# Performance work log

Measured on AMD Instinct MI355X. Metric: run time of the kernel, lower is better.

Reference implementation:

```python
import jax, jax.numpy as jnp
import numpy as np

DEC_LEN = 64  # matches init_kwargs dec_len
B, T = 64, 8192


def setup_inputs() -> dict:
    key = jax.random.key(0)
    k1, k2, k3, k4 = jax.random.split(key, 4)
    return {
        "feats_in": jax.random.normal(k1, (B, T, 1), jnp.float32),
        "X_in": jax.random.normal(k2, (B, T, 1), jnp.float32),
        "feats_out": jax.random.normal(k3, (B, DEC_LEN, 1), jnp.float32),
        "X_out": jax.random.normal(k4, (B, DEC_LEN, 1), jnp.float32),
    }


def reference(feats_in, X_in, feats_out, X_out):
    L = DEC_LEN
    n_win = X_in.shape[1] - L            # number of sliding windows (T - dec_len)
    x = X_in[..., 0]                     # [B, T]
    y = X_out[..., 0]                    # [B, L]
    # all sliding windows via gather: [n_win, L] index -> [B, n_win, L]
    win_idx = jnp.arange(n_win)[:, None] + jnp.arange(L)[None, :]
    windows = x[:, win_idx]              # [B, n_win, L]
    # per-window mean squared distance to the target window
    dists = jnp.mean((windows - y[:, None, :]) ** 2, axis=2)  # [B, n_win]
    start = jnp.argmin(dists, axis=1)    # [B]
    gidx = start[:, None] + jnp.arange(L)[None, :]            # [B, L]
    mean_out = jnp.take_along_axis(x, gidx, axis=1)[..., None]  # [B, L, 1]
    return mean_out
```

## Files before the change

### kernel.cpp

```cpp
#include <hip/hip_runtime.h>
#include <hip/hip_bf16.h>

constexpr int B_SZ  = 64;
constexpr int T_SZ  = 8192;
constexpr int L_SZ  = 64;
constexpr int NWIN  = T_SZ - L_SZ;

__global__ __launch_bounds__(256)
void window_match_kernel(const float* __restrict__ X_in,
                         const float* __restrict__ X_out,
                         float* __restrict__ out)
{
    __shared__ float xs[T_SZ];
    __shared__ float ys[L_SZ];
    __shared__ unsigned long long wred[4];
    __shared__ int win_start;

    const int b   = blockIdx.x;
    const int tid = threadIdx.x;

    const float4* xg  = reinterpret_cast<const float4*>(X_in + (size_t)b * T_SZ);
    float4*       xs4 = reinterpret_cast<float4*>(xs);
    #pragma unroll
    for (int i = 0; i < T_SZ / 4 / 256; ++i)
        xs4[tid + i * 256] = xg[tid + i * 256];

    if (tid < L_SZ) ys[tid] = X_out[(size_t)b * L_SZ + tid];
    __syncthreads();

    float y[L_SZ];
    #pragma unroll
    for (int j = 0; j < L_SZ; ++j) y[j] = ys[j];

    unsigned long long best = ~0ull;

    for (int k = 0; k < 8; ++k) {
        const int s0 = 4 * tid + 1024 * k;
        if (s0 < NWIN) {
            float xv[68];
            const float4* p = reinterpret_cast<const float4*>(xs + s0);
            #pragma unroll
            for (int i = 0; i < 17; ++i) {
                float4 v = p[i];
                xv[4 * i + 0] = v.x;
                xv[4 * i + 1] = v.y;
                xv[4 * i + 2] = v.z;
                xv[4 * i + 3] = v.w;
            }
            #pragma unroll
            for (int w = 0; w < 4; ++w) {
                float d = 0.0f;
                #pragma unroll
                for (int j = 0; j < L_SZ; ++j) {
                    const float t = xv[w + j] - y[j];
                    d = fmaf(t, t, d);
                }
                const unsigned long long key =
                    ((unsigned long long)__float_as_uint(d) << 32) |
                    (unsigned int)(s0 + w);
                best = key < best ? key : best;
            }
        }
    }

    #pragma unroll
    for (int off = 32; off > 0; off >>= 1) {
        const unsigned long long o = __shfl_down(best, off, 64);
        best = o < best ? o : best;
    }
    const int lane = tid & 63;
    const int wv   = tid >> 6;
    if (lane == 0) wred[wv] = best;
    __syncthreads();
    if (tid == 0) {
        unsigned long long m = wred[0];
        m = wred[1] < m ? wred[1] : m;
        m = wred[2] < m ? wred[2] : m;
        m = wred[3] < m ? wred[3] : m;
        win_start = (int)(m & 0xffffffffu);
    }
    __syncthreads();

    if (tid < L_SZ)
        out[(size_t)b * L_SZ + tid] = xs[win_start + tid];
}

extern "C" void kernel_launch(void* const* d_in, const int* in_sizes, int n_in,
                              void* d_out, int out_size, void* d_ws, size_t ws_size,
                              hipStream_t stream) {
    const float* X_in  = (const float*)d_in[1];
    const float* X_out = (const float*)d_in[3];
    float* out = (float*)d_out;

    window_match_kernel<<<B_SZ, 256, 0, stream>>>(X_in, X_out, out);
}
```

Measured before the change: 73.48 us.

## Split each batch's window search across four blocks with second reduction kernel

The sliding-window search for each batch row is divided into four quarter-ranges, each handled by its own block that stages only its slice plus halo in shared memory and writes a packed (distance, index) key to workspace. A second small kernel reduces the four keys per batch and gathers the winning window from global memory. This raises the grid from 64 to 256 blocks so more compute units are busy, at the cost of an extra kernel launch and a workspace round-trip.

Measured after the change: 65.05 us. 11.5% less time.

```diff
diff --git a/kernel.cpp b/kernel.cpp
--- a/kernel.cpp
+++ b/kernel.cpp
@@ -5,25 +5,29 @@
 constexpr int T_SZ  = 8192;
 constexpr int L_SZ  = 64;
 constexpr int NWIN  = T_SZ - L_SZ;
+constexpr int NQ    = 4;
+constexpr int QW    = NWIN / NQ;
+constexpr int STAGE = QW + L_SZ;
 
 __global__ __launch_bounds__(256)
-void window_match_kernel(const float* __restrict__ X_in,
-                         const float* __restrict__ X_out,
-                         float* __restrict__ out)
+void window_match_partial(const float* __restrict__ X_in,
+                          const float* __restrict__ X_out,
+                          unsigned long long* __restrict__ ws_keys)
 {
-    __shared__ float xs[T_SZ];
+    __shared__ float xs[STAGE + 16];
     __shared__ float ys[L_SZ];
     __shared__ unsigned long long wred[4];
-    __shared__ int win_start;
 
-    const int b   = blockIdx.x;
+    const int bq  = blockIdx.x;
+    const int b   = bq >> 2;
+    const int q   = bq & 3;
     const int tid = threadIdx.x;
+    const int base = q * QW;
 
-    const float4* xg  = reinterpret_cast<const float4*>(X_in + (size_t)b * T_SZ);
+    const float4* xg  = reinterpret_cast<const float4*>(X_in + (size_t)b * T_SZ + base);
     float4*       xs4 = reinterpret_cast<float4*>(xs);
-    #pragma unroll
-    for (int i = 0; i < T_SZ / 4 / 256; ++i)
-        xs4[tid + i * 256] = xg[tid + i * 256];
+    for (int i = tid; i < STAGE / 4; i += 256)
+        xs4[i] = xg[i];
 
     if (tid < L_SZ) ys[tid] = X_out[(size_t)b * L_SZ + tid];
     __syncthreads();
@@ -34,9 +38,10 @@
 
     unsigned long long best = ~0ull;
 
-    for (int k = 0; k < 8; ++k) {
+    #pragma unroll
+    for (int k = 0; k < 2; ++k) {
         const int s0 = 4 * tid + 1024 * k;
-        if (s0 < NWIN) {
+        if (s0 < QW) {
             float xv[68];
             const float4* p = reinterpret_cast<const float4*>(xs + s0);
             #pragma unroll
@@ -57,7 +62,7 @@
                 }
                 const unsigned long long key =
                     ((unsigned long long)__float_as_uint(d) << 32) |
-                    (unsigned int)(s0 + w);
+                    (unsigned int)(base + s0 + w);
                 best = key < best ? key : best;
             }
         }
@@ -68,21 +73,33 @@
         const unsigned long long o = __shfl_down(best, off, 64);
         best = o < best ? o : best;
     }
-    const int lane = tid & 63;
-    const int wv   = tid >> 6;
-    if (lane == 0) wred[wv] = best;
+    if ((tid & 63) == 0) wred[tid >> 6] = best;
     __syncthreads();
     if (tid == 0) {
         unsigned long long m = wred[0];
         m = wred[1] < m ? wred[1] : m;
         m = wred[2] < m ? wred[2] : m;
         m = wred[3] < m ? wred[3] : m;
-        win_start = (int)(m & 0xffffffffu);
+        ws_keys[bq] = m;
     }
-    __syncthreads();
+}
 
-    if (tid < L_SZ)
-        out[(size_t)b * L_SZ + tid] = xs[win_start + tid];
+__global__ __launch_bounds__(64)
+void window_match_gather(const float* __restrict__ X_in,
+                         const unsigned long long* __restrict__ ws_keys,
+                         float* __restrict__ out)
+{
+    const int b   = blockIdx.x;
+    const int tid = threadIdx.x;
+
+    unsigned long long m = ws_keys[b * NQ + 0];
+    #pragma unroll
+    for (int qq = 1; qq < NQ; ++qq) {
+        const unsigned long long o = ws_keys[b * NQ + qq];
+        m = o < m ? o : m;
+    }
+    const int s = (int)(m & 0xffffffffu);
+    out[(size_t)b * L_SZ + tid] = X_in[(size_t)b * T_SZ + s + tid];
 }
 
 extern "C" void kernel_launch(void* const* d_in, const int* in_sizes, int n_in,
@@ -91,6 +108,8 @@
     const float* X_in  = (const float*)d_in[1];
     const float* X_out = (const float*)d_in[3];
     float* out = (float*)d_out;
+    unsigned long long* ws_keys = (unsigned long long*)d_ws;
 
-    window_match_kernel<<<B_SZ, 256, 0, stream>>>(X_in, X_out, out);
+    window_match_partial<<<B_SZ * NQ, 256, 0, stream>>>(X_in, X_out, ws_keys);
+    window_match_gather<<<B_SZ, 64, 0, stream>>>(X_in, ws_keys, out);
 }
```
